# Kernel tuning notes

Measured on AMD Instinct MI355X. Metric: run time of the kernel, lower is better.

Reference implementation:

```python
import jax, jax.numpy as jnp
import numpy as np

B, NA, T, NV, D = 24, 50, 10, 196, 512


def setup_inputs() -> dict:
    key = jax.random.key(0)
    k1, k2 = jax.random.split(key)
    return {
        "audio_feats": jax.random.normal(k1, (B, NA, D), dtype=jnp.float32),
        "visual_feats": jax.random.normal(k2, (B, T, NV, D), dtype=jnp.float32),
        "temperature": jnp.float32(2.5),
        "scale_factor": jnp.float32(2.5),
        "threshold": jnp.float32(-2.5),
    }


def _l2norm(x):
    # F.normalize(dim=-1): x / max(||x||, 1e-12)
    n = jnp.sqrt(jnp.sum(x * x, axis=-1, keepdims=True))
    return x / jnp.maximum(n, 1e-12)


def reference(audio_feats, visual_feats, temperature, scale_factor, threshold):
    b = audio_feats.shape[0]
    a = _l2norm(audio_feats)          # (B,Na,D)
    v = _l2norm(visual_feats)         # (B,T,Nv,D)
    # all-pairs token similarities: (B,B,Na,T,Nv)
    sims = jnp.einsum('xad,ytvd->xyatv', a, v) / temperature

    # aggregate_temporal_similarities
    th = jax.nn.sigmoid(threshold)
    max_vis = jnp.max(sims, axis=-1)            # (B,B,Na,T)
    raw_diff = max_vis - th
    sel = jax.nn.relu(raw_diff) * scale_factor  # selection strength
    weighted_sum = jnp.sum(max_vis * sel, axis=-1)   # over T
    weights_sum = jnp.sum(sel, axis=-1)
    token_sims = weighted_sum / jnp.maximum(weights_sum, 1e-6)
    clip_sims = jnp.mean(token_sims, axis=-1)   # (B,B)
    fraction_selected = jnp.mean((raw_diff > 0).astype(jnp.float32))

    # InfoNCE
    idx = jnp.arange(b)
    losses_a2v = -jax.nn.log_softmax(clip_sims, axis=1)[idx, idx]
    losses_v2a = -jax.nn.log_softmax(clip_sims.T, axis=1)[idx, idx]
    contrastive_loss = jnp.mean(losses_a2v + losses_v2a) / 2

    # regularization
    neg = jnp.clip(sims, -20.0, 0.0)
    l_nonneg = jnp.mean(neg * neg)
    temp_low = jnp.maximum(-jnp.log(temperature), 0.0) ** 2   # log(1)=0
    temp_high = jnp.maximum(jnp.log(temperature) - jnp.log(4.0), 0.0) ** 2
    l_cal = temp_low + temp_high
    l_threshold = jnp.maximum(th - 0.9, 0.0) ** 2 + jnp.maximum(0.1 - th, 0.0) ** 2
    l_scale = jnp.maximum(scale_factor - 20.0, 0.0) ** 2 + jnp.maximum(1.0 - scale_factor, 0.0) ** 2
    reg_loss = 0.15 * l_nonneg + 2.0 * l_cal + 0.1 * l_threshold + 0.1 * l_scale

    # selection reward on positive pairs (diagonal)
    pos_diffs = raw_diff[idx, idx]                       # (B,Na,T)
    sel_ratio = (jnp.tanh(20.0 * pos_diffs) + 1.0) / 2.0
    selection_reward = -0.1 * jnp.log1p(jnp.mean(sel_ratio))

    total_loss = selection_reward + contrastive_loss + reg_loss
    return (total_loss, contrastive_loss, reg_loss, fraction_selected, selection_reward)
```

## Files before the change

kernel.cpp:

```cpp
#include <hip/hip_runtime.h>
#include <math.h>

#define B_   24
#define NA_  50
#define T_   10
#define NV_  196
#define D_   512
#define M_   1200
#define MPAD 1280
#define NVP  224
#define YT_  240
#define VROWS (YT_ * NVP)

typedef __bf16 bf16x8 __attribute__((ext_vector_type(8)));
typedef float  f32x4  __attribute__((ext_vector_type(4)));
typedef unsigned short ushort8 __attribute__((ext_vector_type(8)));

__device__ __forceinline__ unsigned short f2bf(float f) {
    unsigned u = __float_as_uint(f);
    u += 0x7FFF + ((u >> 16) & 1);
    return (unsigned short)(u >> 16);
}

__device__ __forceinline__ void gload16(const void* g, void* l) {
    __builtin_amdgcn_global_load_lds(
        (const __attribute__((address_space(1))) unsigned int*)g,
        (__attribute__((address_space(3))) unsigned int*)l, 16, 0, 0);
}

__global__ void normconvA_kernel(const float* __restrict__ a,
                                 const float* __restrict__ tempPtr,
                                 unsigned short* __restrict__ Abf) {
    int w = threadIdx.x >> 6, lane = threadIdx.x & 63;
    int row = blockIdx.x * 4 + w;
    if (row >= MPAD) return;
    ushort8* dst = (ushort8*)(Abf + (size_t)row * D_ + lane * 8);
    if (row < M_) {
        const float* p = a + (size_t)row * D_ + lane * 8;
        float4 u = *(const float4*)p;
        float4 v = *(const float4*)(p + 4);
        float s = u.x*u.x + u.y*u.y + u.z*u.z + u.w*u.w
                + v.x*v.x + v.y*v.y + v.z*v.z + v.w*v.w;
        #pragma unroll
        for (int off = 32; off; off >>= 1) s += __shfl_xor(s, off, 64);
        float sc = 1.0f / (fmaxf(sqrtf(s), 1e-12f) * tempPtr[0]);
        ushort8 o;
        o[0]=f2bf(u.x*sc); o[1]=f2bf(u.y*sc); o[2]=f2bf(u.z*sc); o[3]=f2bf(u.w*sc);
        o[4]=f2bf(v.x*sc); o[5]=f2bf(v.y*sc); o[6]=f2bf(v.z*sc); o[7]=f2bf(v.w*sc);
        *dst = o;
    } else {
        ushort8 z = (ushort8)0;
        *dst = z;
    }
}

__global__ void normconvV_kernel(const float* __restrict__ vf,
                                 unsigned short* __restrict__ Vbf) {
    int w = threadIdx.x >> 6, lane = threadIdx.x & 63;
    int row = blockIdx.x * 4 + w;
    if (row >= VROWS) return;
    int yt = row / NVP, vv = row - yt * NVP;
    ushort8* dst = (ushort8*)(Vbf + (size_t)row * D_ + lane * 8);
    if (vv < NV_) {
        const float* p = vf + ((size_t)yt * NV_ + vv) * D_ + lane * 8;
        float4 u = *(const float4*)p;
        float4 v = *(const float4*)(p + 4);
        float s = u.x*u.x + u.y*u.y + u.z*u.z + u.w*u.w
                + v.x*v.x + v.y*v.y + v.z*v.z + v.w*v.w;
        #pragma unroll
        for (int off = 32; off; off >>= 1) s += __shfl_xor(s, off, 64);
        float sc = 1.0f / fmaxf(sqrtf(s), 1e-12f);
        ushort8 o;
        o[0]=f2bf(u.x*sc); o[1]=f2bf(u.y*sc); o[2]=f2bf(u.z*sc); o[3]=f2bf(u.w*sc);
        o[4]=f2bf(v.x*sc); o[5]=f2bf(v.y*sc); o[6]=f2bf(v.z*sc); o[7]=f2bf(v.w*sc);
        *dst = o;
    } else {
        ushort8 z = (ushort8)0;
        *dst = z;
    }
}

__global__ __launch_bounds__(256) void simred_kernel(
    const unsigned short* __restrict__ Abf, const unsigned short* __restrict__ Vbf,
    float* __restrict__ maxvis, float* __restrict__ accNonneg)
{
    __shared__ __align__(16) unsigned char lds[8192 + 14336];
    __shared__ float maxred[2][128];
    __shared__ float redbuf[4];

    const int tid  = threadIdx.x;
    const int lane = tid & 63;
    const int w    = tid >> 6;
    const int lrow = lane >> 2;
    const int lcol = lane & 3;
    const int q    = lane >> 4;
    const int m16  = lane & 15;
    const int wr   = w & 1;
    const int wc   = w >> 1;
    const int rowA0 = blockIdx.x * 128;
    const int yt    = blockIdx.y;
    const size_t vRow0 = (size_t)yt * NVP;

    const unsigned short* gp[6];
    const unsigned char*  lp[6];
    int nun = 0;
    for (int u = w; u < 22; u += 4) {
        if (u < 8) gp[nun] = Abf + ((size_t)(rowA0 + u * 16 + lrow)) * D_ + lcol * 8;
        else       gp[nun] = Vbf + (vRow0 + (size_t)((u - 8) * 16 + lrow)) * D_ + lcol * 8;
        lp[nun] = lds + u * 1024;
        ++nun;
    }

    const unsigned char* aP[4];
    const unsigned char* bP[7];
    #pragma unroll
    for (int i = 0; i < 4; ++i) aP[i] = lds + (size_t)(wr * 64 + i * 16 + m16) * 64 + q * 16;
    #pragma unroll
    for (int j = 0; j < 7; ++j) bP[j] = lds + 8192 + (size_t)(wc * 112 + j * 16 + m16) * 64 + q * 16;

    f32x4 acc[4][7];
    #pragma unroll
    for (int i = 0; i < 4; ++i)
        #pragma unroll
        for (int j = 0; j < 7; ++j) acc[i][j] = (f32x4)0.0f;

    for (int c = 0; c < 16; ++c) {
        const int kc = c * 32;
        __syncthreads();
        #pragma unroll 6
        for (int i = 0; i < 6; ++i)
            if (i < nun) gload16(gp[i] + kc, (void*)lp[i]);
        __syncthreads();
        bf16x8 af[4], bfr[7];
        #pragma unroll
        for (int i = 0; i < 4; ++i) af[i] = *(const bf16x8*)aP[i];
        #pragma unroll
        for (int j = 0; j < 7; ++j) bfr[j] = *(const bf16x8*)bP[j];
        #pragma unroll
        for (int i = 0; i < 4; ++i)
            #pragma unroll
            for (int j = 0; j < 7; ++j)
                acc[i][j] = __builtin_amdgcn_mfma_f32_16x16x32_bf16(af[i], bfr[j], acc[i][j], 0, 0, 0);
    }

    float cs = 0.0f;
    #pragma unroll
    for (int i = 0; i < 4; ++i)
        #pragma unroll
        for (int j = 0; j < 7; ++j)
            #pragma unroll
            for (int r = 0; r < 4; ++r) {
                float v = acc[i][j][r];
                float cv = fminf(fmaxf(v, -20.0f), 0.0f);
                cs += cv * cv;
            }
    #pragma unroll
    for (int off = 32; off; off >>= 1) cs += __shfl_xor(cs, off, 64);
    if (lane == 0) redbuf[w] = cs;

    bool colv[7];
    #pragma unroll
    for (int j = 0; j < 7; ++j) colv[j] = (wc * 112 + j * 16 + m16) < NV_;
    #pragma unroll
    for (int i = 0; i < 4; ++i) {
        float mx[4] = {-3e38f, -3e38f, -3e38f, -3e38f};
        #pragma unroll
        for (int j = 0; j < 7; ++j)
            #pragma unroll
            for (int r = 0; r < 4; ++r)
                mx[r] = fmaxf(mx[r], colv[j] ? acc[i][j][r] : -3e38f);
        #pragma unroll
        for (int r = 0; r < 4; ++r) {
            float mm = mx[r];
            #pragma unroll
            for (int off = 1; off <= 8; off <<= 1) mm = fmaxf(mm, __shfl_xor(mm, off, 64));
            if (m16 == 0) maxred[wc][wr * 64 + i * 16 + q * 4 + r] = mm;
        }
    }
    __syncthreads();
    if (tid == 0) atomicAdd(accNonneg, redbuf[0] + redbuf[1] + redbuf[2] + redbuf[3]);
    if (tid < 128) {
        float mm = fmaxf(maxred[0][tid], maxred[1][tid]);
        int R = rowA0 + tid;
        if (R < M_) {
            int x = R / NA_, a = R - x * NA_;
            int y = yt / T_, t = yt - y * T_;
            maxvis[(((size_t)x * B_ + y) * NA_ + a) * T_ + t] = mm;
        }
    }
}

__global__ void aggregate_kernel(const float* __restrict__ maxvis,
                                 const float* __restrict__ thrPtr,
                                 const float* __restrict__ scalePtr,
                                 float* __restrict__ clipSims,
                                 float* __restrict__ accFrac,
                                 float* __restrict__ accSel)
{
    int xy = blockIdx.x;
    int x = xy / B_, y = xy % B_;
    int a = threadIdx.x;
    float th    = 1.0f / (1.0f + expf(-thrPtr[0]));
    float scale = scalePtr[0];
    float token = 0.0f, cnt = 0.0f, selsum = 0.0f;
    if (a < NA_) {
        const float* p = maxvis + (((size_t)x * B_ + y) * NA_ + a) * T_;
        float ws = 0.0f, ss = 0.0f;
        #pragma unroll
        for (int t = 0; t < T_; ++t) {
            float mv  = p[t];
            float rd  = mv - th;
            float sel = fmaxf(rd, 0.0f) * scale;
            ws += mv * sel;
            ss += sel;
            if (rd > 0.0f) cnt += 1.0f;
            if (x == y) selsum += 0.5f * (tanhf(20.0f * rd) + 1.0f);
        }
        token = ws / fmaxf(ss, 1e-6f);
    }
    #pragma unroll
    for (int off = 32; off; off >>= 1) {
        token  += __shfl_xor(token,  off, 64);
        cnt    += __shfl_xor(cnt,    off, 64);
        selsum += __shfl_xor(selsum, off, 64);
    }
    if (threadIdx.x == 0) {
        clipSims[x * B_ + y] = token / (float)NA_;
        atomicAdd(accFrac, cnt);
        if (x == y) atomicAdd(accSel, selsum);
    }
}

__global__ void finalize_kernel(const float* __restrict__ clipSims,
                                const float* __restrict__ accs,
                                const float* __restrict__ tempPtr,
                                const float* __restrict__ scalePtr,
                                const float* __restrict__ thrPtr,
                                float* __restrict__ out)
{
    __shared__ float cs[B_ * B_];
    int tid = threadIdx.x;
    for (int i = tid; i < B_ * B_; i += 64) cs[i] = clipSims[i];
    __syncthreads();
    float lsum = 0.0f;
    if (tid < B_) {
        int i = tid;
        float m = -1e30f;
        for (int j = 0; j < B_; ++j) m = fmaxf(m, cs[i * B_ + j]);
        float e = 0.0f;
        for (int j = 0; j < B_; ++j) e += expf(cs[i * B_ + j] - m);
        float la = m + logf(e) - cs[i * B_ + i];
        float m2 = -1e30f;
        for (int j = 0; j < B_; ++j) m2 = fmaxf(m2, cs[j * B_ + i]);
        float e2 = 0.0f;
        for (int j = 0; j < B_; ++j) e2 += expf(cs[j * B_ + i] - m2);
        float lv = m2 + logf(e2) - cs[i * B_ + i];
        lsum = la + lv;
    }
    #pragma unroll
    for (int off = 32; off; off >>= 1) lsum += __shfl_xor(lsum, off, 64);
    if (tid == 0) {
        float contrastive = lsum / (float)B_ * 0.5f;
        float temp = tempPtr[0], scl = scalePtr[0];
        float th = 1.0f / (1.0f + expf(-thrPtr[0]));
        float l_nonneg = accs[0] / 56448000.0f;
        float logt = logf(temp);
        float tl  = fmaxf(-logt, 0.0f);
        float thi = fmaxf(logt - logf(4.0f), 0.0f);
        float l_cal = tl * tl + thi * thi;
        float t1 = fmaxf(th - 0.9f, 0.0f), t2 = fmaxf(0.1f - th, 0.0f);
        float l_thr = t1 * t1 + t2 * t2;
        float s1 = fmaxf(scl - 20.0f, 0.0f), s2 = fmaxf(1.0f - scl, 0.0f);
        float l_scale = s1 * s1 + s2 * s2;
        float reg = 0.15f * l_nonneg + 2.0f * l_cal + 0.1f * l_thr + 0.1f * l_scale;
        float frac   = accs[1] / 288000.0f;
        float selrew = -0.1f * log1pf(accs[2] / 12000.0f);
        out[0] = selrew + contrastive + reg;
        out[1] = contrastive;
        out[2] = reg;
        out[3] = frac;
        out[4] = selrew;
    }
}

extern "C" void kernel_launch(void* const* d_in, const int* in_sizes, int n_in,
                              void* d_out, int out_size, void* d_ws, size_t ws_size,
                              hipStream_t stream) {
    const float* audio  = (const float*)d_in[0];
    const float* visual = (const float*)d_in[1];
    const float* temp   = (const float*)d_in[2];
    const float* scale  = (const float*)d_in[3];
    const float* thr    = (const float*)d_in[4];
    float* out = (float*)d_out;

    unsigned char* wsb = (unsigned char*)d_ws;
    unsigned short* Abf = (unsigned short*)wsb;
    unsigned short* Vbf = (unsigned short*)(wsb + 1310720);
    float* maxvis   = (float*)(wsb + 1310720 + 55050240);
    float* clipSims = (float*)(wsb + 1310720 + 55050240 + 1152000);
    float* accs     = clipSims + 576;

    hipMemsetAsync(accs, 0, 3 * sizeof(float), stream);

    normconvA_kernel<<<MPAD / 4, 256, 0, stream>>>(audio, temp, Abf);
    normconvV_kernel<<<VROWS / 4, 256, 0, stream>>>(visual, Vbf);

    dim3 grid(MPAD / 128, YT_);
    simred_kernel<<<grid, 256, 0, stream>>>(Abf, Vbf, maxvis, accs);

    aggregate_kernel<<<B_ * B_, 64, 0, stream>>>(maxvis, thr, scale, clipSims, accs + 1, accs + 2);
    finalize_kernel<<<1, 64, 0, stream>>>(clipSims, accs, temp, scale, thr, out);
}
```

Baseline: 287.5 us.

## Double-buffer LDS tiles and XOR-swizzle layout in similarity GEMM

Splits LDS into two buffers so the global-to-LDS loads for the next K chunk are issued before the MFMA work on the current chunk, removing one barrier per iteration. It also XOR-swizzles the 16-byte column position by row, applied consistently on the global source address and on the LDS read offsets, to reduce LDS bank conflicts on fragment reads. LDS use per block doubles to about 45KB, which may lower occupancy.

```diff
diff --git a/kernel.cpp b/kernel.cpp
--- a/kernel.cpp
+++ b/kernel.cpp
@@ -80,11 +80,13 @@
     }
 }
 
+#define BUFB 22528u
+
 __global__ __launch_bounds__(256) void simred_kernel(
     const unsigned short* __restrict__ Abf, const unsigned short* __restrict__ Vbf,
     float* __restrict__ maxvis, float* __restrict__ accNonneg)
 {
-    __shared__ __align__(16) unsigned char lds[8192 + 14336];
+    __shared__ __align__(16) unsigned char lds[2 * BUFB];
     __shared__ float maxred[2][128];
     __shared__ float redbuf[4];
 
@@ -101,22 +103,25 @@
     const int yt    = blockIdx.y;
     const size_t vRow0 = (size_t)yt * NVP;
 
+    const int scol = lcol ^ ((lrow >> 1) & 3);
     const unsigned short* gp[6];
-    const unsigned char*  lp[6];
+    unsigned loff[6];
     int nun = 0;
     for (int u = w; u < 22; u += 4) {
-        if (u < 8) gp[nun] = Abf + ((size_t)(rowA0 + u * 16 + lrow)) * D_ + lcol * 8;
-        else       gp[nun] = Vbf + (vRow0 + (size_t)((u - 8) * 16 + lrow)) * D_ + lcol * 8;
-        lp[nun] = lds + u * 1024;
+        if (u < 8) gp[nun] = Abf + ((size_t)(rowA0 + u * 16 + lrow)) * D_ + scol * 8;
+        else       gp[nun] = Vbf + (vRow0 + (size_t)((u - 8) * 16 + lrow)) * D_ + scol * 8;
+        loff[nun] = (unsigned)u * 1024u;
         ++nun;
     }
 
-    const unsigned char* aP[4];
-    const unsigned char* bP[7];
-    #pragma unroll
-    for (int i = 0; i < 4; ++i) aP[i] = lds + (size_t)(wr * 64 + i * 16 + m16) * 64 + q * 16;
-    #pragma unroll
-    for (int j = 0; j < 7; ++j) bP[j] = lds + 8192 + (size_t)(wc * 112 + j * 16 + m16) * 64 + q * 16;
+    const unsigned rsw = (unsigned)((m16 >> 1) & 3) * 16u;
+    unsigned aoff[4], boff[7];
+    #pragma unroll
+    for (int i = 0; i < 4; ++i)
+        aoff[i] = (unsigned)(wr * 64 + i * 16 + m16) * 64u + (((unsigned)q * 16u) ^ rsw);
+    #pragma unroll
+    for (int j = 0; j < 7; ++j)
+        boff[j] = 8192u + (unsigned)(wc * 112 + j * 16 + m16) * 64u + (((unsigned)q * 16u) ^ rsw);
 
     f32x4 acc[4][7];
     #pragma unroll
@@ -124,23 +129,31 @@
         #pragma unroll
         for (int j = 0; j < 7; ++j) acc[i][j] = (f32x4)0.0f;
 
+    #pragma unroll 6
+    for (int i = 0; i < 6; ++i)
+        if (i < nun) gload16(gp[i], (void*)(lds + loff[i]));
+    __syncthreads();
+
     for (int c = 0; c < 16; ++c) {
-        const int kc = c * 32;
-        __syncthreads();
-        #pragma unroll 6
-        for (int i = 0; i < 6; ++i)
-            if (i < nun) gload16(gp[i] + kc, (void*)lp[i]);
-        __syncthreads();
+        const unsigned char* buf = lds + (unsigned)(c & 1) * BUFB;
+        if (c < 15) {
+            const int kc2 = (c + 1) * 32;
+            const unsigned nb = (unsigned)((c + 1) & 1) * BUFB;
+            #pragma unroll 6
+            for (int i = 0; i < 6; ++i)
+                if (i < nun) gload16(gp[i] + kc2, (void*)(lds + nb + loff[i]));
+        }
         bf16x8 af[4], bfr[7];
         #pragma unroll
-        for (int i = 0; i < 4; ++i) af[i] = *(const bf16x8*)aP[i];
-        #pragma unroll
-        for (int j = 0; j < 7; ++j) bfr[j] = *(const bf16x8*)bP[j];
+        for (int i = 0; i < 4; ++i) af[i] = *(const bf16x8*)(buf + aoff[i]);
+        #pragma unroll
+        for (int j = 0; j < 7; ++j) bfr[j] = *(const bf16x8*)(buf + boff[j]);
         #pragma unroll
         for (int i = 0; i < 4; ++i)
             #pragma unroll
             for (int j = 0; j < 7; ++j)
                 acc[i][j] = __builtin_amdgcn_mfma_f32_16x16x32_bf16(af[i], bfr[j], acc[i][j], 0, 0, 0);
+        __syncthreads();
     }
 
     float cs = 0.0f;
```

New measurement: 351.3 us. 22.2% more time.

## Load MFMA operands directly from global memory instead of staging through LDS

Applied to the files above, without the earlier changes.

The GEMM main loop stops staging A and V tiles into shared memory with global_load_lds plus two barriers per K-chunk. Each wave now loads its bf16 fragments straight from global memory, the K loop is fully unrolled, and launch bounds request two blocks per CU. This removes the barriers and LDS round trips, but each wave re-fetches the operands that other waves share, so the kernel relies on L1/L2 caching and may use more global bandwidth and registers.

```diff
diff --git a/kernel.cpp b/kernel.cpp
--- a/kernel.cpp
+++ b/kernel.cpp
@@ -20,12 +20,6 @@
     unsigned u = __float_as_uint(f);
     u += 0x7FFF + ((u >> 16) & 1);
     return (unsigned short)(u >> 16);
-}
-
-__device__ __forceinline__ void gload16(const void* g, void* l) {
-    __builtin_amdgcn_global_load_lds(
-        (const __attribute__((address_space(1))) unsigned int*)g,
-        (__attribute__((address_space(3))) unsigned int*)l, 16, 0, 0);
 }
 
 __global__ void normconvA_kernel(const float* __restrict__ a,
@@ -80,19 +74,16 @@
     }
 }
 
-__global__ __launch_bounds__(256) void simred_kernel(
+__global__ __launch_bounds__(256, 2) void simred_kernel(
     const unsigned short* __restrict__ Abf, const unsigned short* __restrict__ Vbf,
     float* __restrict__ maxvis, float* __restrict__ accNonneg)
 {
-    __shared__ __align__(16) unsigned char lds[8192 + 14336];
     __shared__ float maxred[2][128];
     __shared__ float redbuf[4];
 
     const int tid  = threadIdx.x;
     const int lane = tid & 63;
     const int w    = tid >> 6;
-    const int lrow = lane >> 2;
-    const int lcol = lane & 3;
     const int q    = lane >> 4;
     const int m16  = lane & 15;
     const int wr   = w & 1;
@@ -101,22 +92,14 @@
     const int yt    = blockIdx.y;
     const size_t vRow0 = (size_t)yt * NVP;
 
-    const unsigned short* gp[6];
-    const unsigned char*  lp[6];
-    int nun = 0;
-    for (int u = w; u < 22; u += 4) {
-        if (u < 8) gp[nun] = Abf + ((size_t)(rowA0 + u * 16 + lrow)) * D_ + lcol * 8;
-        else       gp[nun] = Vbf + (vRow0 + (size_t)((u - 8) * 16 + lrow)) * D_ + lcol * 8;
-        lp[nun] = lds + u * 1024;
-        ++nun;
-    }
-
-    const unsigned char* aP[4];
-    const unsigned char* bP[7];
-    #pragma unroll
-    for (int i = 0; i < 4; ++i) aP[i] = lds + (size_t)(wr * 64 + i * 16 + m16) * 64 + q * 16;
-    #pragma unroll
-    for (int j = 0; j < 7; ++j) bP[j] = lds + 8192 + (size_t)(wc * 112 + j * 16 + m16) * 64 + q * 16;
+    const unsigned short* pA[4];
+    const unsigned short* pB[7];
+    #pragma unroll
+    for (int i = 0; i < 4; ++i)
+        pA[i] = Abf + ((size_t)(rowA0 + wr * 64 + i * 16 + m16)) * D_ + q * 8;
+    #pragma unroll
+    for (int j = 0; j < 7; ++j)
+        pB[j] = Vbf + (vRow0 + (size_t)(wc * 112 + j * 16 + m16)) * D_ + q * 8;
 
     f32x4 acc[4][7];
     #pragma unroll
@@ -124,23 +107,18 @@
         #pragma unroll
         for (int j = 0; j < 7; ++j) acc[i][j] = (f32x4)0.0f;
 
+    #pragma unroll
     for (int c = 0; c < 16; ++c) {
-        const int kc = c * 32;
-        __syncthreads();
-        #pragma unroll 6
-        for (int i = 0; i < 6; ++i)
-            if (i < nun) gload16(gp[i] + kc, (void*)lp[i]);
-        __syncthreads();
-        bf16x8 af[4], bfr[7];
-        #pragma unroll
-        for (int i = 0; i < 4; ++i) af[i] = *(const bf16x8*)aP[i];
-        #pragma unroll
-        for (int j = 0; j < 7; ++j) bfr[j] = *(const bf16x8*)bP[j];
+        bf16x8 af[4], bv[7];
+        #pragma unroll
+        for (int i = 0; i < 4; ++i) af[i] = *(const bf16x8*)(pA[i] + c * 32);
+        #pragma unroll
+        for (int j = 0; j < 7; ++j) bv[j] = *(const bf16x8*)(pB[j] + c * 32);
         #pragma unroll
         for (int i = 0; i < 4; ++i)
             #pragma unroll
             for (int j = 0; j < 7; ++j)
-                acc[i][j] = __builtin_amdgcn_mfma_f32_16x16x32_bf16(af[i], bfr[j], acc[i][j], 0, 0, 0);
+                acc[i][j] = __builtin_amdgcn_mfma_f32_16x16x32_bf16(af[i], bv[j], acc[i][j], 0, 0, 0);
     }
 
     float cs = 0.0f;
```

Measured after the change: 407.6 us. 1.42x slower.
